# Kernel optimization log

Measured on AMD Instinct MI355X. Metric: run time of the kernel, lower is better.

The kernel has to match this reference:

```python
import jax, jax.numpy as jnp
import numpy as np

NODELEN = 17949
N_NODES = 512
N_EDGES = 4096
H2 = 768
EMB = 128
IN_DIM = 2 * NODELEN


def _seg_mean(h, src, dst, n):
    # gather neighbor features and mean-reduce per destination node
    msg = h[src]                                   # [E, F]
    s = jax.ops.segment_sum(msg, dst, num_segments=n)
    deg = jax.ops.segment_sum(jnp.ones((src.shape[0],), h.dtype), dst, num_segments=n)
    return s / jnp.maximum(deg, 1.0)[:, None]


def setup_inputs() -> dict:
    key = jax.random.key(0)
    ks = jax.random.split(key, 12)
    s = 0.02
    return {
        "x": jax.random.normal(ks[0], (N_NODES, NODELEN), jnp.float32),
        "edge_src": jax.random.randint(ks[1], (N_EDGES,), 0, N_NODES),
        "edge_dst": jax.random.randint(ks[2], (N_EDGES,), 0, N_NODES),
        "W_e2": jax.random.normal(ks[3], (H2, IN_DIM), jnp.float32) * s,
        "b_e2": jnp.zeros((H2,), jnp.float32),
        "W_e3": jax.random.normal(ks[4], (EMB, H2), jnp.float32) * s,
        "b_e3": jnp.zeros((EMB,), jnp.float32),
        "W_d1": jax.random.normal(ks[5], (H2, EMB), jnp.float32) * s,
        "b_d1": jnp.zeros((H2,), jnp.float32),
        "W_d3": jax.random.normal(ks[6], (IN_DIM, H2), jnp.float32) * s,
        "b_d3": jnp.zeros((IN_DIM,), jnp.float32),
    }


def reference(x, edge_src, edge_dst, W_e2, b_e2, W_e3, b_e3, W_d1, b_d1, W_d3, b_d3):
    n = x.shape[0]
    # depth-2 recursive GraphSAGE mean aggregation; agg[0]=0 after each hop
    h1 = _seg_mean(x, edge_src, edge_dst, n).at[:, 0].set(0.0)
    h2 = _seg_mean(h1, edge_src, edge_dst, n).at[:, 0].set(0.0)
    emb = jnp.concatenate([x, h2], axis=1)           # [N, 2*NODELEN]
    emb = emb.at[:, 0].set(0.0).at[:, NODELEN].set(0.0)
    # AutoEncoder (eval mode: dropout is identity)
    h = jax.nn.relu(emb @ W_e2.T + b_e2)
    encoded = h @ W_e3.T + b_e3
    h = jax.nn.relu(encoded @ W_d1.T + b_d1)
    decoded = h @ W_d3.T + b_d3
    return encoded, decoded
```

## Files before the change

kernel.cpp:

```cpp
#include <hip/hip_runtime.h>
#include <hip/hip_bf16.h>

#define NODELEN 17949
#define NN 512
#define NE 4096
#define H2 768
#define EMB 128
#define IN_DIM (2 * NODELEN)
#define KP1 35904
#define KITERS1 561
#define SPLITS 16
#define KCHUNK1 36

#define BM 128
#define BN 128
#define BK 64
#define LDT (BK + 8)

typedef __bf16 bf16x8 __attribute__((ext_vector_type(8)));
typedef float f32x4 __attribute__((ext_vector_type(4)));


__global__ void k_zero_int(int* p, int n) {
    int i = blockIdx.x * 256 + threadIdx.x;
    if (i < n) p[i] = 0;
}

__global__ void k_deg(const int* __restrict__ dst, int* __restrict__ cnt) {
    int e = blockIdx.x * 256 + threadIdx.x;
    if (e < NE) atomicAdd(&cnt[dst[e]], 1);
}

__global__ void k_scan(const int* __restrict__ cnt, int* __restrict__ offs,
                       float* __restrict__ invdeg) {
    __shared__ int s[NN];
    int t = threadIdx.x;
    int c = cnt[t];
    s[t] = c;
    int cd = c > 1 ? c : 1;
    invdeg[t] = 1.0f / (float)cd;
    __syncthreads();
    for (int d = 1; d < NN; d <<= 1) {
        int add = (t >= d) ? s[t - d] : 0;
        __syncthreads();
        s[t] += add;
        __syncthreads();
    }
    offs[t + 1] = s[t];
    if (t == 0) offs[0] = 0;
}

__global__ void k_fill(const int* __restrict__ src, const int* __restrict__ dst,
                       const int* __restrict__ offs, int* __restrict__ cursor,
                       int* __restrict__ csr) {
    int e = blockIdx.x * 256 + threadIdx.x;
    if (e < NE) {
        int d = dst[e];
        int pos = offs[d] + atomicAdd(&cursor[d], 1);
        csr[pos] = src[e];
    }
}

__global__ void k_agg(const float* __restrict__ in, float* __restrict__ out,
                      const int* __restrict__ csr, const int* __restrict__ offs,
                      const float* __restrict__ invdeg) {
    int f = blockIdx.x * 256 + threadIdx.x;
    int n = blockIdx.y;
    if (f >= NODELEN) return;
    int e0 = offs[n], e1 = offs[n + 1];
    float s = 0.f;
    for (int e = e0; e < e1; ++e) {
        s += in[(size_t)csr[e] * NODELEN + f];
    }
    float v = (f == 0) ? 0.f : s * invdeg[n];
    out[(size_t)n * NODELEN + f] = v;
}

__global__ void k_emb(const float* __restrict__ x, const float* __restrict__ h2,
                      __bf16* __restrict__ embb) {
    int c = blockIdx.x * 256 + threadIdx.x;
    int n = blockIdx.y;
    if (c >= KP1) return;
    float v;
    if (c < NODELEN) v = (c == 0) ? 0.f : x[(size_t)n * NODELEN + c];
    else if (c < IN_DIM) v = h2[(size_t)n * NODELEN + (c - NODELEN)];
    else v = 0.f;
    embb[(size_t)n * KP1 + c] = (__bf16)v;
}


template <bool PARTIAL, bool BIAS>
__global__ __launch_bounds__(256) void gemm_bf16(
        const __bf16* __restrict__ A, int lda,
        const float* __restrict__ B, int ldb,
        int Nvalid, int Kvalid, int kIters, int kChunk,
        float* __restrict__ C, int ldc,
        const float* __restrict__ bias,
        float* __restrict__ partials) {
    __shared__ __align__(16) __bf16 As[BM][LDT];
    __shared__ __align__(16) __bf16 Bs[BN][LDT];

    const int tid = threadIdx.x;
    const int m0 = blockIdx.x * BM;
    const int n0 = blockIdx.y * BN;
    const int z = blockIdx.z;

    int it0 = z * kChunk;
    int it1 = it0 + kChunk;
    if (it1 > kIters) it1 = kIters;

    const int wave = tid >> 6;
    const int lane = tid & 63;
    const int wm = (wave & 1) * 64;
    const int wn = (wave >> 1) * 64;
    const int fl = lane & 15;
    const int fq = lane >> 4;

    const int srow = tid >> 1;
    const int spart = tid & 1;

    f32x4 acc[4][4] = {};

    const int bn = n0 + srow;
    const bool nok = bn < Nvalid;

    for (int it = it0; it < it1; ++it) {
        int k0 = it * BK;

        {
            const uint4* Ag = (const uint4*)(A + (size_t)(m0 + srow) * lda + k0 + spart * 32);
            uint4 av[4];
#pragma unroll
            for (int i = 0; i < 4; ++i) av[i] = Ag[i];
#pragma unroll
            for (int i = 0; i < 4; ++i)
                *(uint4*)&As[srow][spart * 32 + i * 8] = av[i];
        }
        {
            __align__(16) __bf16 bl[32];
            if (nok && (k0 + BK) <= Kvalid) {
                const float2* Bg = (const float2*)(B + (size_t)bn * ldb + k0 + spart * 32);
                float2 f[16];
#pragma unroll
                for (int j = 0; j < 16; ++j) f[j] = Bg[j];
#pragma unroll
                for (int j = 0; j < 16; ++j) {
                    bl[2 * j] = (__bf16)f[j].x;
                    bl[2 * j + 1] = (__bf16)f[j].y;
                }
            } else {
#pragma unroll
                for (int j = 0; j < 32; ++j) {
                    int kk = k0 + spart * 32 + j;
                    float v = (nok && kk < Kvalid) ? B[(size_t)bn * ldb + kk] : 0.f;
                    bl[j] = (__bf16)v;
                }
            }
#pragma unroll
            for (int q = 0; q < 4; ++q)
                *(uint4*)&Bs[srow][spart * 32 + q * 8] = *(uint4*)&bl[q * 8];
        }
        __syncthreads();

#pragma unroll
        for (int ks = 0; ks < 2; ++ks) {
            int kk = ks * 32 + fq * 8;
            bf16x8 af[4], bf[4];
#pragma unroll
            for (int i = 0; i < 4; ++i)
                af[i] = *(const bf16x8*)&As[wm + i * 16 + fl][kk];
#pragma unroll
            for (int j = 0; j < 4; ++j)
                bf[j] = *(const bf16x8*)&Bs[wn + j * 16 + fl][kk];
#pragma unroll
            for (int i = 0; i < 4; ++i)
#pragma unroll
                for (int j = 0; j < 4; ++j)
                    acc[i][j] = __builtin_amdgcn_mfma_f32_16x16x32_bf16(
                        af[i], bf[j], acc[i][j], 0, 0, 0);
        }
        __syncthreads();
    }

#pragma unroll
    for (int i = 0; i < 4; ++i) {
#pragma unroll
        for (int j = 0; j < 4; ++j) {
#pragma unroll
            for (int r = 0; r < 4; ++r) {
                int m = m0 + wm + i * 16 + fq * 4 + r;
                int n = n0 + wn + j * 16 + fl;
                float v = acc[i][j][r];
                if (PARTIAL) {
                    partials[((size_t)z * (BM * 4) + m) * H2 + n] = v;
                } else {
                    if (n < Nvalid) {
                        if (BIAS) v += bias[n];
                        C[(size_t)m * ldc + n] = v;
                    }
                }
            }
        }
    }
}

__global__ void k_reduce(const float* __restrict__ partials,
                         const float* __restrict__ bias, float* __restrict__ h) {
    int idx = blockIdx.x * 256 + threadIdx.x;
    if (idx >= NN * H2) return;
    float s = 0.f;
#pragma unroll
    for (int z = 0; z < SPLITS; ++z) s += partials[(size_t)z * NN * H2 + idx];
    s += bias[idx % H2];
    h[idx] = s > 0.f ? s : 0.f;
}

__global__ void k_enc(const float* __restrict__ h, const float* __restrict__ W,
                      const float* __restrict__ b, float* __restrict__ out) {
    int m = blockIdx.x, e = threadIdx.x;
    const float4* hr = (const float4*)(h + (size_t)m * H2);
    const float4* wr = (const float4*)(W + (size_t)e * H2);
    float s = 0.f;
#pragma unroll 4
    for (int i = 0; i < H2 / 4; ++i) {
        float4 a = hr[i];
        float4 w = wr[i];
        s += a.x * w.x + a.y * w.y + a.z * w.z + a.w * w.w;
    }
    out[(size_t)m * EMB + e] = s + b[e];
}

__global__ void k_dec1(const float* __restrict__ enc, const float* __restrict__ W,
                       const float* __restrict__ b, __bf16* __restrict__ hd) {
    int m = blockIdx.x;
    __shared__ float er[EMB];
    if (threadIdx.x < EMB) er[threadIdx.x] = enc[(size_t)m * EMB + threadIdx.x];
    __syncthreads();
    for (int j = threadIdx.x; j < H2; j += 256) {
        const float4* wr = (const float4*)(W + (size_t)j * EMB);
        float s = 0.f;
#pragma unroll
        for (int i = 0; i < EMB / 4; ++i) {
            float4 w = wr[i];
            s += w.x * er[4 * i] + w.y * er[4 * i + 1] + w.z * er[4 * i + 2] +
                 w.w * er[4 * i + 3];
        }
        float v = s + b[j];
        hd[(size_t)m * H2 + j] = (__bf16)(v > 0.f ? v : 0.f);
    }
}


extern "C" void kernel_launch(void* const* d_in, const int* in_sizes, int n_in,
                              void* d_out, int out_size, void* d_ws, size_t ws_size,
                              hipStream_t stream) {
    const float* x = (const float*)d_in[0];
    const int* esrc = (const int*)d_in[1];
    const int* edst = (const int*)d_in[2];
    const float* W_e2 = (const float*)d_in[3];
    const float* b_e2 = (const float*)d_in[4];
    const float* W_e3 = (const float*)d_in[5];
    const float* b_e3 = (const float*)d_in[6];
    const float* W_d1 = (const float*)d_in[7];
    const float* b_d1 = (const float*)d_in[8];
    const float* W_d3 = (const float*)d_in[9];
    const float* b_d3 = (const float*)d_in[10];
    float* out = (float*)d_out;

    char* w = (char*)d_ws;
    auto alloc = [&](size_t bytes) {
        char* p = w;
        w += (bytes + 255) & ~(size_t)255;
        return p;
    };
    float* partials = (float*)alloc((size_t)SPLITS * NN * H2 * 4);
    float* h1 = (float*)alloc((size_t)NN * NODELEN * 4);
    float* h2 = (float*)alloc((size_t)NN * NODELEN * 4);
    __bf16* embb = (__bf16*)alloc((size_t)NN * KP1 * 2);
    float* h = (float*)alloc((size_t)NN * H2 * 4);
    __bf16* hd_b = (__bf16*)alloc((size_t)NN * H2 * 2);
    int* cnt = (int*)alloc(NN * 4);
    int* cursor = (int*)alloc(NN * 4);
    int* offs = (int*)alloc((NN + 1) * 4);
    int* csr = (int*)alloc(NE * 4);
    float* invdeg = (float*)alloc(NN * 4);

    k_zero_int<<<4, 256, 0, stream>>>(cnt, NN);
    k_zero_int<<<4, 256, 0, stream>>>(cursor, NN);
    k_deg<<<NE / 256, 256, 0, stream>>>(edst, cnt);
    k_scan<<<1, NN, 0, stream>>>(cnt, offs, invdeg);
    k_fill<<<NE / 256, 256, 0, stream>>>(esrc, edst, offs, cursor, csr);

    dim3 gagg((NODELEN + 255) / 256, NN);
    k_agg<<<gagg, 256, 0, stream>>>(x, h1, csr, offs, invdeg);
    k_agg<<<gagg, 256, 0, stream>>>(h1, h2, csr, offs, invdeg);

    dim3 gemb((KP1 + 255) / 256, NN);
    k_emb<<<gemb, 256, 0, stream>>>(x, h2, embb);

    dim3 g1(NN / BM, H2 / BN, SPLITS);
    gemm_bf16<true, false><<<g1, 256, 0, stream>>>(
        embb, KP1, W_e2, IN_DIM, H2, IN_DIM, KITERS1, KCHUNK1,
        (float*)nullptr, 0, (const float*)nullptr, partials);

    k_reduce<<<(NN * H2) / 256, 256, 0, stream>>>(partials, b_e2, h);

    k_enc<<<NN, EMB, 0, stream>>>(h, W_e3, b_e3, out);

    k_dec1<<<NN, 256, 0, stream>>>(out, W_d1, b_d1, hd_b);

    dim3 g4(NN / BM, (IN_DIM + BN - 1) / BN, 1);
    gemm_bf16<false, true><<<g4, 256, 0, stream>>>(
        hd_b, H2, W_d3, H2, IN_DIM, H2, H2 / BK, H2 / BK,
        out + (size_t)NN * EMB, IN_DIM, b_d3, (float*)nullptr);
}
```

Baseline: 671.9 us.

## Replace two-hop gather aggregation with dense A² GEMM and pre-converted bf16 weights

The two per-edge gather passes are replaced by a dense row-normalized adjacency matrix built with atomics. It is squared in a small kernel, and h2 is computed as A² @ x through the MFMA GEMM, whose epilogue writes bf16 straight into the embedding buffer and zeroes column 0. W_e2 is converted once per call to padded bf16, so the large encoder GEMM loads bf16 B tiles instead of converting fp32 per M-block. Split-K is changed from 16 to 24, and scratch buffers are aliased into the partials region. Costs and risks: an extra transpose and conversion pass, extra bf16 rounding of A² and x, and reliance on the ordering of the aliased scratch memory.

```diff
diff --git a/kernel.cpp b/kernel.cpp
--- a/kernel.cpp
+++ b/kernel.cpp
@@ -9,8 +9,8 @@
 #define IN_DIM (2 * NODELEN)
 #define KP1 35904
 #define KITERS1 561
-#define SPLITS 16
-#define KCHUNK1 36
+#define SPLITS 24
+#define KCHUNK1 24
 
 #define BM 128
 #define BN 128
@@ -26,77 +26,113 @@
     if (i < n) p[i] = 0;
 }
 
+__global__ void k_zero_f4(float4* p, int n4) {
+    int i = blockIdx.x * 256 + threadIdx.x;
+    if (i < n4) p[i] = make_float4(0.f, 0.f, 0.f, 0.f);
+}
+
 __global__ void k_deg(const int* __restrict__ dst, int* __restrict__ cnt) {
     int e = blockIdx.x * 256 + threadIdx.x;
     if (e < NE) atomicAdd(&cnt[dst[e]], 1);
 }
 
-__global__ void k_scan(const int* __restrict__ cnt, int* __restrict__ offs,
-                       float* __restrict__ invdeg) {
-    __shared__ int s[NN];
-    int t = threadIdx.x;
-    int c = cnt[t];
-    s[t] = c;
-    int cd = c > 1 ? c : 1;
-    invdeg[t] = 1.0f / (float)cd;
-    __syncthreads();
-    for (int d = 1; d < NN; d <<= 1) {
-        int add = (t >= d) ? s[t - d] : 0;
-        __syncthreads();
-        s[t] += add;
-        __syncthreads();
-    }
-    offs[t + 1] = s[t];
-    if (t == 0) offs[0] = 0;
-}
-
-__global__ void k_fill(const int* __restrict__ src, const int* __restrict__ dst,
-                       const int* __restrict__ offs, int* __restrict__ cursor,
-                       int* __restrict__ csr) {
+__global__ void k_invdeg(const int* __restrict__ cnt, float* __restrict__ invdeg) {
+    int i = blockIdx.x * 256 + threadIdx.x;
+    if (i < NN) {
+        int c = cnt[i];
+        invdeg[i] = 1.0f / (float)(c > 1 ? c : 1);
+    }
+}
+
+__global__ void k_scatter(const int* __restrict__ src, const int* __restrict__ dst,
+                          const float* __restrict__ invdeg, float* __restrict__ A) {
     int e = blockIdx.x * 256 + threadIdx.x;
     if (e < NE) {
         int d = dst[e];
-        int pos = offs[d] + atomicAdd(&cursor[d], 1);
-        csr[pos] = src[e];
-    }
-}
-
-__global__ void k_agg(const float* __restrict__ in, float* __restrict__ out,
-                      const int* __restrict__ csr, const int* __restrict__ offs,
-                      const float* __restrict__ invdeg) {
-    int f = blockIdx.x * 256 + threadIdx.x;
-    int n = blockIdx.y;
-    if (f >= NODELEN) return;
-    int e0 = offs[n], e1 = offs[n + 1];
-    float s = 0.f;
-    for (int e = e0; e < e1; ++e) {
-        s += in[(size_t)csr[e] * NODELEN + f];
-    }
-    float v = (f == 0) ? 0.f : s * invdeg[n];
-    out[(size_t)n * NODELEN + f] = v;
-}
-
-__global__ void k_emb(const float* __restrict__ x, const float* __restrict__ h2,
-                      __bf16* __restrict__ embb) {
+        atomicAdd(&A[(size_t)d * NN + src[e]], invdeg[d]);
+    }
+}
+
+__global__ void k_a2(const float* __restrict__ A, __bf16* __restrict__ A2b) {
+    int i = blockIdx.x;
+    int t = threadIdx.x;
+    __shared__ float row[NN];
+    row[t] = A[(size_t)i * NN + t];
+    row[t + 256] = A[(size_t)i * NN + 256 + t];
+    __syncthreads();
+    float a0 = 0.f, a1 = 0.f;
+    for (int s = 0; s < NN; ++s) {
+        float a = row[s];
+        if (a != 0.f) {
+            a0 += a * A[(size_t)s * NN + t];
+            a1 += a * A[(size_t)s * NN + 256 + t];
+        }
+    }
+    A2b[(size_t)i * NN + t] = (__bf16)a0;
+    A2b[(size_t)i * NN + 256 + t] = (__bf16)a1;
+}
+
+__global__ void k_xt(const float* __restrict__ x, __bf16* __restrict__ xT) {
+    __shared__ float t[64][65];
+    int f0 = blockIdx.x * 64, s0 = blockIdx.y * 64;
+    int tx = threadIdx.x & 63, ty = threadIdx.x >> 6;
+#pragma unroll
+    for (int r = 0; r < 16; ++r) {
+        int f = f0 + tx;
+        t[ty * 16 + r][tx] = (f < NODELEN) ? x[(size_t)(s0 + ty * 16 + r) * NODELEN + f] : 0.f;
+    }
+    __syncthreads();
+#pragma unroll
+    for (int r = 0; r < 16; ++r) {
+        int f = f0 + ty * 16 + r;
+        if (f < NODELEN) xT[(size_t)f * NN + s0 + tx] = (__bf16)t[tx][ty * 16 + r];
+    }
+}
+
+__global__ void k_embx(const float* __restrict__ x, __bf16* __restrict__ embb) {
     int c = blockIdx.x * 256 + threadIdx.x;
     int n = blockIdx.y;
-    if (c >= KP1) return;
-    float v;
-    if (c < NODELEN) v = (c == 0) ? 0.f : x[(size_t)n * NODELEN + c];
-    else if (c < IN_DIM) v = h2[(size_t)n * NODELEN + (c - NODELEN)];
-    else v = 0.f;
-    embb[(size_t)n * KP1 + c] = (__bf16)v;
-}
-
-
-template <bool PARTIAL, bool BIAS>
-__global__ __launch_bounds__(256) void gemm_bf16(
+    if (c < NODELEN) {
+        float v = (c == 0) ? 0.f : x[(size_t)n * NODELEN + c];
+        embb[(size_t)n * KP1 + c] = (__bf16)v;
+    } else {
+        int cc = c - NODELEN;
+        if (cc < KP1 - IN_DIM) embb[(size_t)n * KP1 + IN_DIM + cc] = (__bf16)0.f;
+    }
+}
+
+__global__ void k_cvt_we2(const float* __restrict__ W, __bf16* __restrict__ Wb) {
+    const int C8 = KP1 / 8;
+    int idx = blockIdx.x * 256 + threadIdx.x;
+    if (idx >= H2 * C8) return;
+    int r = idx / C8, c8 = (idx % C8) * 8;
+    __align__(16) __bf16 o[8];
+    if (c8 + 8 <= IN_DIM) {
+        const float2* p = (const float2*)(W + (size_t)r * IN_DIM + c8);
+#pragma unroll
+        for (int j = 0; j < 4; ++j) {
+            float2 f = p[j];
+            o[2 * j] = (__bf16)f.x;
+            o[2 * j + 1] = (__bf16)f.y;
+        }
+    } else {
+#pragma unroll
+        for (int j = 0; j < 8; ++j) {
+            int c = c8 + j;
+            o[j] = (c < IN_DIM) ? (__bf16)W[(size_t)r * IN_DIM + c] : (__bf16)0.f;
+        }
+    }
+    *(uint4*)&Wb[(size_t)r * KP1 + c8] = *(uint4*)o;
+}
+
+
+template <int EPI, bool BF16B>
+__global__ __launch_bounds__(256) void gemm_k(
         const __bf16* __restrict__ A, int lda,
-        const float* __restrict__ B, int ldb,
-        int Nvalid, int Kvalid, int kIters, int kChunk,
-        float* __restrict__ C, int ldc,
-        const float* __restrict__ bias,
-        float* __restrict__ partials) {
+        const void* __restrict__ Bv, int ldb,
+        int Nvalid, int kIters, int kChunk,
+        float* __restrict__ Cf, int ldc, const float* __restrict__ bias,
+        __bf16* __restrict__ Cb) {
     __shared__ __align__(16) __bf16 As[BM][LDT];
     __shared__ __align__(16) __bf16 Bs[BN][LDT];
 
@@ -136,25 +172,36 @@
             for (int i = 0; i < 4; ++i)
                 *(uint4*)&As[srow][spart * 32 + i * 8] = av[i];
         }
-        {
+        if (BF16B) {
+            uint4 bv[4];
+            if (nok) {
+                const uint4* Bg = (const uint4*)((const __bf16*)Bv + (size_t)bn * ldb + k0 + spart * 32);
+#pragma unroll
+                for (int i = 0; i < 4; ++i) bv[i] = Bg[i];
+            } else {
+#pragma unroll
+                for (int i = 0; i < 4; ++i) bv[i] = make_uint4(0, 0, 0, 0);
+            }
+#pragma unroll
+            for (int i = 0; i < 4; ++i)
+                *(uint4*)&Bs[srow][spart * 32 + i * 8] = bv[i];
+        } else {
             __align__(16) __bf16 bl[32];
-            if (nok && (k0 + BK) <= Kvalid) {
-                const float2* Bg = (const float2*)(B + (size_t)bn * ldb + k0 + spart * 32);
-                float2 f[16];
-#pragma unroll
-                for (int j = 0; j < 16; ++j) f[j] = Bg[j];
-#pragma unroll
-                for (int j = 0; j < 16; ++j) {
-                    bl[2 * j] = (__bf16)f[j].x;
-                    bl[2 * j + 1] = (__bf16)f[j].y;
+            if (nok) {
+                const float4* Bg = (const float4*)((const float*)Bv + (size_t)bn * ldb + k0 + spart * 32);
+                float4 f[8];
+#pragma unroll
+                for (int j = 0; j < 8; ++j) f[j] = Bg[j];
+#pragma unroll
+                for (int j = 0; j < 8; ++j) {
+                    bl[4 * j] = (__bf16)f[j].x;
+                    bl[4 * j + 1] = (__bf16)f[j].y;
+                    bl[4 * j + 2] = (__bf16)f[j].z;
+                    bl[4 * j + 3] = (__bf16)f[j].w;
                 }
             } else {
 #pragma unroll
-                for (int j = 0; j < 32; ++j) {
-                    int kk = k0 + spart * 32 + j;
-                    float v = (nok && kk < Kvalid) ? B[(size_t)bn * ldb + kk] : 0.f;
-                    bl[j] = (__bf16)v;
-                }
+                for (int j = 0; j < 32; ++j) bl[j] = (__bf16)0.f;
             }
 #pragma unroll
             for (int q = 0; q < 4; ++q)
@@ -191,13 +238,13 @@
                 int m = m0 + wm + i * 16 + fq * 4 + r;
                 int n = n0 + wn + j * 16 + fl;
                 float v = acc[i][j][r];
-                if (PARTIAL) {
-                    partials[((size_t)z * (BM * 4) + m) * H2 + n] = v;
+                if (EPI == 0) {
+                    Cf[((size_t)z * NN + m) * H2 + n] = v;
+                } else if (EPI == 1) {
+                    if (n < Nvalid) Cf[(size_t)m * ldc + n] = v + bias[n];
                 } else {
-                    if (n < Nvalid) {
-                        if (BIAS) v += bias[n];
-                        C[(size_t)m * ldc + n] = v;
-                    }
+                    if (n < Nvalid)
+                        Cb[(size_t)m * KP1 + NODELEN + n] = (n == 0) ? (__bf16)0.f : (__bf16)v;
                 }
             }
         }
@@ -210,7 +257,7 @@
     if (idx >= NN * H2) return;
     float s = 0.f;
 #pragma unroll
-    for (int z = 0; z < SPLITS; ++z) s += partials[(size_t)z * NN * H2 + idx];
+    for (int zz = 0; zz < SPLITS; ++zz) s += partials[(size_t)zz * NN * H2 + idx];
     s += bias[idx % H2];
     h[idx] = s > 0.f ? s : 0.f;
 }
@@ -273,35 +320,41 @@
         w += (bytes + 255) & ~(size_t)255;
         return p;
     };
-    float* partials = (float*)alloc((size_t)SPLITS * NN * H2 * 4);
-    float* h1 = (float*)alloc((size_t)NN * NODELEN * 4);
-    float* h2 = (float*)alloc((size_t)NN * NODELEN * 4);
     __bf16* embb = (__bf16*)alloc((size_t)NN * KP1 * 2);
+    __bf16* We2b = (__bf16*)alloc((size_t)H2 * KP1 * 2);
+    char* uni = (char*)alloc((size_t)SPLITS * NN * H2 * 4);
+    __bf16* xTb = (__bf16*)uni;
+    float* Adj = (float*)(uni + (size_t)17952 * NN * 2);
+    __bf16* A2b = (__bf16*)((char*)Adj + (size_t)NN * NN * 4);
+    int* cnt = (int*)((char*)A2b + (size_t)NN * NN * 2);
+    float* invdeg = (float*)((char*)cnt + 2048);
+    float* partials = (float*)uni;
     float* h = (float*)alloc((size_t)NN * H2 * 4);
     __bf16* hd_b = (__bf16*)alloc((size_t)NN * H2 * 2);
-    int* cnt = (int*)alloc(NN * 4);
-    int* cursor = (int*)alloc(NN * 4);
-    int* offs = (int*)alloc((NN + 1) * 4);
-    int* csr = (int*)alloc(NE * 4);
-    float* invdeg = (float*)alloc(NN * 4);
-
-    k_zero_int<<<4, 256, 0, stream>>>(cnt, NN);
-    k_zero_int<<<4, 256, 0, stream>>>(cursor, NN);
+
+    k_zero_int<<<2, 256, 0, stream>>>(cnt, NN);
+    k_zero_f4<<<256, 256, 0, stream>>>((float4*)Adj, NN * NN / 4);
     k_deg<<<NE / 256, 256, 0, stream>>>(edst, cnt);
-    k_scan<<<1, NN, 0, stream>>>(cnt, offs, invdeg);
-    k_fill<<<NE / 256, 256, 0, stream>>>(esrc, edst, offs, cursor, csr);
-
-    dim3 gagg((NODELEN + 255) / 256, NN);
-    k_agg<<<gagg, 256, 0, stream>>>(x, h1, csr, offs, invdeg);
-    k_agg<<<gagg, 256, 0, stream>>>(h1, h2, csr, offs, invdeg);
-
-    dim3 gemb((KP1 + 255) / 256, NN);
-    k_emb<<<gemb, 256, 0, stream>>>(x, h2, embb);
+    k_invdeg<<<2, 256, 0, stream>>>(cnt, invdeg);
+    k_scatter<<<NE / 256, 256, 0, stream>>>(esrc, edst, invdeg, Adj);
+    k_a2<<<NN, 256, 0, stream>>>(Adj, A2b);
+
+    dim3 gxt((NODELEN + 63) / 64, NN / 64);
+    k_xt<<<gxt, 256, 0, stream>>>(x, xTb);
+    dim3 gex((NODELEN + 255) / 256, NN);
+    k_embx<<<gex, 256, 0, stream>>>(x, embb);
+
+    dim3 gh2(NN / BM, (NODELEN + BN - 1) / BN, 1);
+    gemm_k<2, true><<<gh2, 256, 0, stream>>>(
+        A2b, NN, xTb, NN, NODELEN, NN / BK, NN / BK,
+        (float*)nullptr, 0, (const float*)nullptr, embb);
+
+    k_cvt_we2<<<(H2 * (KP1 / 8) + 255) / 256, 256, 0, stream>>>(W_e2, We2b);
 
     dim3 g1(NN / BM, H2 / BN, SPLITS);
-    gemm_bf16<true, false><<<g1, 256, 0, stream>>>(
-        embb, KP1, W_e2, IN_DIM, H2, IN_DIM, KITERS1, KCHUNK1,
-        (float*)nullptr, 0, (const float*)nullptr, partials);
+    gemm_k<0, true><<<g1, 256, 0, stream>>>(
+        embb, KP1, We2b, KP1, H2, KITERS1, KCHUNK1,
+        partials, 0, (const float*)nullptr, (__bf16*)nullptr);
 
     k_reduce<<<(NN * H2) / 256, 256, 0, stream>>>(partials, b_e2, h);
 
@@ -310,7 +363,7 @@
     k_dec1<<<NN, 256, 0, stream>>>(out, W_d1, b_d1, hd_b);
 
     dim3 g4(NN / BM, (IN_DIM + BN - 1) / BN, 1);
-    gemm_bf16<false, true><<<g4, 256, 0, stream>>>(
-        hd_b, H2, W_d3, H2, IN_DIM, H2, H2 / BK, H2 / BK,
-        out + (size_t)NN * EMB, IN_DIM, b_d3, (float*)nullptr);
-}
+    gemm_k<1, false><<<g4, 256, 0, stream>>>(
+        hd_b, H2, W_d3, H2, IN_DIM, H2 / BK, H2 / BK,
+        out + (size_t)NN * EMB, IN_DIM, b_d3, (__bf16*)nullptr);
+}
```

After: 591.7 us. -11.9%, faster.
